# Kernel optimization log

Measured on AMD Instinct MI355X. Metric: run time of the kernel, lower is better.

Reference implementation:

```python
import jax, jax.numpy as jnp
import numpy as np

T, H, I, R, Z, K = 4096, 1024, 512, 32, 8, 4
E = R + Z
CAP = 768  # per-expert capacity; mean load = T*K/E = 409.6, CAP is ~18 sigma above mean


def setup_inputs() -> dict:
    key = jax.random.key(0)
    k1, k2, k3, k4, k5 = jax.random.split(key, 5)
    hidden_states = jax.random.normal(k1, (T, H), jnp.float32)
    top_k_index = jax.random.randint(k2, (T, K), 0, E).astype(jnp.int64)
    top_k_weights = jax.random.uniform(k3, (T, K), jnp.float32)
    gate_up_proj = jax.random.normal(k4, (E, 2 * I, H), jnp.float32) * 0.02
    down_proj = jax.random.normal(k5, (R, H, I), jnp.float32) * 0.02
    return {
        "hidden_states": hidden_states,
        "top_k_index": top_k_index,
        "top_k_weights": top_k_weights,
        "gate_up_proj": gate_up_proj,
        "down_proj": down_proj,
    }


def reference(hidden_states, top_k_index, top_k_weights, gate_up_proj, down_proj):
    n_tok, h = hidden_states.shape
    k = top_k_index.shape[1]
    n_routed = down_proj.shape[0]
    n_total = gate_up_proj.shape[0]
    A = n_tok * k  # total assignments

    flat_e = top_k_index.reshape(-1).astype(jnp.int32)          # [A]
    flat_t = jnp.repeat(jnp.arange(n_tok, dtype=jnp.int32), k)  # [A]
    flat_w = top_k_weights.reshape(-1)                          # [A]

    # ---- zero experts: weighted identity ----
    zero_w = jnp.sum(jnp.where(top_k_index >= n_routed, top_k_weights, 0.0), axis=1)
    out = hidden_states * zero_w[:, None]

    # ---- routed experts via capacity-buffer grouped GEMM ----
    order = jnp.argsort(flat_e)  # stable sort groups assignments by expert
    se = flat_e[order]
    st = flat_t[order]
    sw = flat_w[order]

    counts = jnp.bincount(flat_e, length=n_total)        # [E]
    starts = jnp.cumsum(counts) - counts                 # exclusive cumsum
    pos = jnp.arange(A, dtype=jnp.int32) - starts[se].astype(jnp.int32)  # slot within expert

    valid = (se < n_routed) & (pos < CAP)
    e_idx = jnp.where(valid, se, 0)
    p_idx = jnp.where(valid, pos, 0)

    xs = jnp.where(valid[:, None], hidden_states[st], 0.0)   # [A,H]
    xbuf = jnp.zeros((n_routed, CAP, h), hidden_states.dtype).at[e_idx, p_idx].add(xs)

    # grouped gated MLP: F.linear(x, W) == x @ W.T with W [out,in]
    gu = jnp.einsum('ech,eoh->eco', xbuf, gate_up_proj[:n_routed])  # [R,CAP,2I]
    gate, up = jnp.split(gu, 2, axis=-1)
    mid = jax.nn.silu(gate) * up                                    # [R,CAP,I]
    ybuf = jnp.einsum('eci,ehi->ech', mid, down_proj)               # [R,CAP,H]

    ya = ybuf[e_idx, p_idx] * jnp.where(valid, sw, 0.0)[:, None]    # [A,H]
    out = out.at[st].add(ya)
    return out
```

## Files before the change

kernel.cpp:

```cpp
#include <hip/hip_runtime.h>
#include <stdint.h>

#define NT 4096
#define HD 1024
#define ID 512
#define RE 32
#define EE 40
#define KT 4
#define CAPACITY 768

typedef __bf16 bf16x8 __attribute__((ext_vector_type(8)));
typedef float f32x4 __attribute__((ext_vector_type(4)));
typedef unsigned int u32x4 __attribute__((ext_vector_type(4)));
typedef unsigned int u32x2 __attribute__((ext_vector_type(2)));
typedef unsigned short u16x4 __attribute__((ext_vector_type(4)));

__device__ __forceinline__ float bf2f(unsigned short u) {
    union { unsigned int i; float f; } v; v.i = ((unsigned int)u) << 16; return v.f;
}
__device__ __forceinline__ unsigned short f2bf(float f) {
    union { float f; unsigned int i; } v; v.f = f;
    unsigned int u = v.i;
    return (unsigned short)((u + 0x7fffu + ((u >> 16) & 1u)) >> 16);
}

__device__ __forceinline__ u32x4 ld8(const void* p, size_t ei, int inF32) {
    if (!inF32) {
        return *(const u32x4*)((const unsigned short*)p + ei);
    } else {
        const float* f = (const float*)p + ei;
        f32x4 a = *(const f32x4*)f;
        f32x4 b = *(const f32x4*)(f + 4);
        u32x4 r;
        r[0] = (unsigned)f2bf(a[0]) | ((unsigned)f2bf(a[1]) << 16);
        r[1] = (unsigned)f2bf(a[2]) | ((unsigned)f2bf(a[3]) << 16);
        r[2] = (unsigned)f2bf(b[0]) | ((unsigned)f2bf(b[1]) << 16);
        r[3] = (unsigned)f2bf(b[2]) | ((unsigned)f2bf(b[3]) << 16);
        return r;
    }
}

typedef __attribute__((address_space(1))) const unsigned int gas_u32;
typedef __attribute__((address_space(3))) unsigned int las_u32;
#define GLL(g, l) __builtin_amdgcn_global_load_lds((gas_u32*)(g), (las_u32*)(l), 16, 0, 0)

__global__ __launch_bounds__(256) void detect_k(const void* __restrict__ X,
                                                const void* __restrict__ idx,
                                                int* __restrict__ flags) {
    __shared__ int sInsane, sOddNZ;
    const int tid = threadIdx.x;
    if (tid == 0) { sInsane = 0; sOddNZ = 0; }
    __syncthreads();
    const unsigned short* xu = (const unsigned short*)X;
    int cnt = 0;
    for (int i = tid; i < 8192; i += 256) {
        int e = (xu[i] >> 7) & 0xFF;
        if (e >= 0x90) cnt++;
    }
    if (cnt) atomicAdd(&sInsane, cnt);
    const int* ip = (const int*)idx;
    int odd = 0;
    for (int i = tid; i < 512; i += 256)
        if ((i & 1) && ip[i] != 0) odd++;
    if (odd) atomicAdd(&sOddNZ, odd);
    __syncthreads();
    if (tid == 0) {
        flags[0] = (sInsane > 64) ? 1 : 0;
        flags[1] = (sOddNZ == 0) ? 1 : 0;
    }
}

__global__ __launch_bounds__(256) void route_k(const int* __restrict__ idx,
                                               const void* __restrict__ wts,
                                               const int* __restrict__ flags,
                                               int* __restrict__ cnt,
                                               float* __restrict__ zw,
                                               int* __restrict__ tok,
                                               float* __restrict__ wslot,
                                               int* __restrict__ smap) {
    int a = blockIdx.x * 256 + threadIdx.x;
    if (a >= NT * KT) return;
    const int isI64 = flags[1];
    const int inF32 = flags[0];
    int e = isI64 ? idx[a << 1] : idx[a];
    float w = inF32 ? ((const float*)wts)[a] : bf2f(((const unsigned short*)wts)[a]);
    int s = -1;
    if (e < RE) {
        int slot = atomicAdd(&cnt[e], 1);
        if (slot < CAPACITY) {
            tok[e * CAPACITY + slot] = a >> 2;
            wslot[e * CAPACITY + slot] = w;
            s = slot;
        }
    } else {
        atomicAdd(&zw[a >> 2], w);
    }
    smap[a] = s;
}

__global__ __launch_bounds__(256) void convert_k(
    const void* __restrict__ X, const void* __restrict__ W1, const void* __restrict__ W2,
    const int* __restrict__ flags, const float* __restrict__ zw,
    unsigned short* __restrict__ Xb, unsigned short* __restrict__ W1b,
    unsigned short* __restrict__ W2b, float* __restrict__ out)
{
    const int inF32 = flags[0];
    const size_t gid = (size_t)blockIdx.x * 256 + threadIdx.x;
    const size_t stride = (size_t)gridDim.x * 256;
    const size_t nx = (size_t)NT * HD / 4;
    const size_t n1 = (size_t)RE * 2 * ID * HD / 4;
    const size_t n2 = (size_t)RE * HD * ID / 4;
    if (inF32) {
        for (size_t i = gid; i < nx; i += stride) {
            f32x4 v = ((const f32x4*)X)[i];
            u32x2 r; r[0] = (unsigned)f2bf(v[0]) | ((unsigned)f2bf(v[1]) << 16);
            r[1] = (unsigned)f2bf(v[2]) | ((unsigned)f2bf(v[3]) << 16);
            ((u32x2*)Xb)[i] = r;
            float z = zw[i >> 8];
            f32x4 o = {z * v[0], z * v[1], z * v[2], z * v[3]};
            ((f32x4*)out)[i] = o;
        }
        for (size_t i = gid; i < n1; i += stride) {
            f32x4 v = ((const f32x4*)W1)[i];
            u32x2 r; r[0] = (unsigned)f2bf(v[0]) | ((unsigned)f2bf(v[1]) << 16);
            r[1] = (unsigned)f2bf(v[2]) | ((unsigned)f2bf(v[3]) << 16);
            ((u32x2*)W1b)[i] = r;
        }
        for (size_t i = gid; i < n2; i += stride) {
            f32x4 v = ((const f32x4*)W2)[i];
            u32x2 r; r[0] = (unsigned)f2bf(v[0]) | ((unsigned)f2bf(v[1]) << 16);
            r[1] = (unsigned)f2bf(v[2]) | ((unsigned)f2bf(v[3]) << 16);
            ((u32x2*)W2b)[i] = r;
        }
    } else {
        for (size_t i = gid; i < nx; i += stride) {
            u32x2 r = ((const u32x2*)X)[i];
            ((u32x2*)Xb)[i] = r;
            float z = zw[i >> 8];
            f32x4 o = {z * bf2f((unsigned short)(r[0] & 0xffffu)),
                       z * bf2f((unsigned short)(r[0] >> 16)),
                       z * bf2f((unsigned short)(r[1] & 0xffffu)),
                       z * bf2f((unsigned short)(r[1] >> 16))};
            ((f32x4*)out)[i] = o;
        }
        for (size_t i = gid; i < n1; i += stride) ((u32x2*)W1b)[i] = ((const u32x2*)W1)[i];
        for (size_t i = gid; i < n2; i += stride) ((u32x2*)W2b)[i] = ((const u32x2*)W2)[i];
    }
}

__global__ __launch_bounds__(256, 2) void gemm1n_k(
    const unsigned short* __restrict__ Xb,
    const unsigned short* __restrict__ W1b,
    const int* __restrict__ cnts,
    const int* __restrict__ tok,
    unsigned short* __restrict__ mid)
{
    const int e = blockIdx.z;
    int cnt = cnts[e]; if (cnt > CAPACITY) cnt = CAPACITY;
    const int m0 = blockIdx.x * 128;
    if (m0 >= cnt) return;
    const int n0 = blockIdx.y * 128;

    __shared__ unsigned short Ash[3 * 4096];
    __shared__ unsigned short Bgs[3 * 4096];
    __shared__ unsigned short Bus[3 * 4096];

    const int tid  = threadIdx.x;
    const int lane = tid & 63;
    const int wv   = tid >> 6;
    const int wm   = wv >> 1, wn = wv & 1;
    const int q    = lane >> 4, ln = lane & 15;

    const int r0 = m0 + lane, r1 = m0 + 64 + lane;
    const int t0 = (r0 < cnt) ? tok[e * CAPACITY + r0] : 0;
    const int t1 = (r1 < cnt) ? tok[e * CAPACITY + r1] : 0;
    const unsigned short* gA0 = Xb + (size_t)t0 * HD + wv * 8;
    const unsigned short* gA1 = Xb + (size_t)t1 * HD + wv * 8;
    const unsigned short* gG0 = W1b + ((size_t)e * 1024 + n0 + lane) * HD + wv * 8;
    const unsigned short* gG1 = gG0 + (size_t)64 * HD;
    const unsigned short* gU0 = W1b + ((size_t)e * 1024 + 512 + n0 + lane) * HD + wv * 8;
    const unsigned short* gU1 = gU0 + (size_t)64 * HD;
    const int l0 = (wv * 128 + 0) * 8;
    const int l1 = (wv * 128 + 64) * 8;

    f32x4 accg[4][4], accu[4][4];
    const f32x4 z4 = {0.f, 0.f, 0.f, 0.f};
    #pragma unroll
    for (int a_ = 0; a_ < 4; a_++)
        #pragma unroll
        for (int b_ = 0; b_ < 4; b_++) { accg[a_][b_] = z4; accu[a_][b_] = z4; }

    #define STAGE1(k0, b) do { \
        GLL(gA0 + (k0), &Ash[(b) * 4096 + l0]); GLL(gA1 + (k0), &Ash[(b) * 4096 + l1]); \
        GLL(gG0 + (k0), &Bgs[(b) * 4096 + l0]); GLL(gG1 + (k0), &Bgs[(b) * 4096 + l1]); \
        GLL(gU0 + (k0), &Bus[(b) * 4096 + l0]); GLL(gU1 + (k0), &Bus[(b) * 4096 + l1]); } while (0)

    STAGE1(0, 0); STAGE1(32, 1); STAGE1(64, 2);

    int bsel = 0;
    for (int t = 0; t < 32; ++t) {
        if (t < 30)       asm volatile("s_waitcnt vmcnt(12)" ::: "memory");
        else if (t == 30) asm volatile("s_waitcnt vmcnt(6)" ::: "memory");
        else              asm volatile("s_waitcnt vmcnt(0)" ::: "memory");
        __builtin_amdgcn_s_barrier();
        __builtin_amdgcn_sched_barrier(0);
        const unsigned short* As = &Ash[bsel * 4096];
        const unsigned short* Gs = &Bgs[bsel * 4096];
        const unsigned short* Us = &Bus[bsel * 4096];
        bf16x8 af[4], bgf[4], buf2[4];
        #pragma unroll
        for (int mt = 0; mt < 4; mt++)
            af[mt] = *(const bf16x8*)&As[(q * 128 + wm * 64 + mt * 16 + ln) * 8];
        #pragma unroll
        for (int nt = 0; nt < 4; nt++) {
            bgf[nt]  = *(const bf16x8*)&Gs[(q * 128 + wn * 64 + nt * 16 + ln) * 8];
            buf2[nt] = *(const bf16x8*)&Us[(q * 128 + wn * 64 + nt * 16 + ln) * 8];
        }
        #pragma unroll
        for (int mt = 0; mt < 4; mt++)
            #pragma unroll
            for (int nt = 0; nt < 4; nt++) {
                accg[mt][nt] = __builtin_amdgcn_mfma_f32_16x16x32_bf16(af[mt], bgf[nt],  accg[mt][nt], 0, 0, 0);
                accu[mt][nt] = __builtin_amdgcn_mfma_f32_16x16x32_bf16(af[mt], buf2[nt], accu[mt][nt], 0, 0, 0);
            }
        asm volatile("s_waitcnt lgkmcnt(0)" ::: "memory");
        __builtin_amdgcn_sched_barrier(0);
        __builtin_amdgcn_s_barrier();
        __builtin_amdgcn_sched_barrier(0);
        if (t < 29) STAGE1((t + 3) * 32, bsel);
        bsel++; if (bsel == 3) bsel = 0;
    }
    #undef STAGE1

    const size_t midBase = (size_t)e * CAPACITY;
    #pragma unroll
    for (int mt = 0; mt < 4; mt++) {
        #pragma unroll
        for (int r = 0; r < 4; r++) {
            int slot = m0 + wm * 64 + mt * 16 + q * 4 + r;
            if (slot < cnt) {
                unsigned short* dst = mid + (midBase + slot) * ID;
                #pragma unroll
                for (int nt = 0; nt < 4; nt++) {
                    int i_col = n0 + wn * 64 + nt * 16 + ln;
                    float gv = accg[mt][nt][r];
                    float uv = accu[mt][nt][r];
                    float sv = gv / (1.f + __expf(-gv));
                    dst[i_col] = f2bf(sv * uv);
                }
            }
        }
    }
}

__global__ __launch_bounds__(256, 2) void gemm2n_k(
    const unsigned short* __restrict__ mid,
    const unsigned short* __restrict__ W2b,
    const int* __restrict__ cnts,
    const int* __restrict__ tok,
    const float* __restrict__ wslot,
    float* __restrict__ out)
{
    const int e = blockIdx.z;
    int cnt = cnts[e]; if (cnt > CAPACITY) cnt = CAPACITY;
    const int m0 = blockIdx.x * 128;
    if (m0 >= cnt) return;
    const int n0 = blockIdx.y * 128;

    __shared__ unsigned short Ash[3 * 4096];
    __shared__ unsigned short Bsh[3 * 4096];

    const int tid  = threadIdx.x;
    const int lane = tid & 63;
    const int wv   = tid >> 6;
    const int wm   = wv >> 1, wn = wv & 1;
    const int q    = lane >> 4, ln = lane & 15;

    const unsigned short* gA0 = mid + ((size_t)e * CAPACITY + m0 + lane) * ID + wv * 8;
    const unsigned short* gA1 = gA0 + (size_t)64 * ID;
    const unsigned short* gB0 = W2b + ((size_t)e * HD + n0 + lane) * ID + wv * 8;
    const unsigned short* gB1 = gB0 + (size_t)64 * ID;
    const int l0 = (wv * 128 + 0) * 8;
    const int l1 = (wv * 128 + 64) * 8;

    f32x4 acc[4][4];
    const f32x4 z4 = {0.f, 0.f, 0.f, 0.f};
    #pragma unroll
    for (int a_ = 0; a_ < 4; a_++)
        #pragma unroll
        for (int b_ = 0; b_ < 4; b_++) acc[a_][b_] = z4;

    #define STAGE2(k0, b) do { \
        GLL(gA0 + (k0), &Ash[(b) * 4096 + l0]); GLL(gA1 + (k0), &Ash[(b) * 4096 + l1]); \
        GLL(gB0 + (k0), &Bsh[(b) * 4096 + l0]); GLL(gB1 + (k0), &Bsh[(b) * 4096 + l1]); } while (0)

    STAGE2(0, 0); STAGE2(32, 1); STAGE2(64, 2);

    int bsel = 0;
    for (int t = 0; t < 16; ++t) {
        if (t < 14)       asm volatile("s_waitcnt vmcnt(8)" ::: "memory");
        else if (t == 14) asm volatile("s_waitcnt vmcnt(4)" ::: "memory");
        else              asm volatile("s_waitcnt vmcnt(0)" ::: "memory");
        __builtin_amdgcn_s_barrier();
        __builtin_amdgcn_sched_barrier(0);
        const unsigned short* As = &Ash[bsel * 4096];
        const unsigned short* Bs = &Bsh[bsel * 4096];
        bf16x8 af[4], bf[4];
        #pragma unroll
        for (int mt = 0; mt < 4; mt++)
            af[mt] = *(const bf16x8*)&As[(q * 128 + wm * 64 + mt * 16 + ln) * 8];
        #pragma unroll
        for (int nt = 0; nt < 4; nt++)
            bf[nt] = *(const bf16x8*)&Bs[(q * 128 + wn * 64 + nt * 16 + ln) * 8];
        #pragma unroll
        for (int mt = 0; mt < 4; mt++)
            #pragma unroll
            for (int nt = 0; nt < 4; nt++)
                acc[mt][nt] = __builtin_amdgcn_mfma_f32_16x16x32_bf16(af[mt], bf[nt], acc[mt][nt], 0, 0, 0);
        asm volatile("s_waitcnt lgkmcnt(0)" ::: "memory");
        __builtin_amdgcn_sched_barrier(0);
        __builtin_amdgcn_s_barrier();
        __builtin_amdgcn_sched_barrier(0);
        if (t < 13) STAGE2((t + 3) * 32, bsel);
        bsel++; if (bsel == 3) bsel = 0;
    }
    #undef STAGE2

    const int base = e * CAPACITY;
    #pragma unroll
    for (int mt = 0; mt < 4; mt++) {
        #pragma unroll
        for (int r = 0; r < 4; r++) {
            int slot = m0 + wm * 64 + mt * 16 + q * 4 + r;
            if (slot < cnt) {
                int tt = tok[base + slot];
                float w = wslot[base + slot];
                float* dst = out + (size_t)tt * HD + n0 + wn * 64 + ln;
                #pragma unroll
                for (int nt = 0; nt < 4; nt++)
                    atomicAdd(dst + nt * 16, w * acc[mt][nt][r]);
            }
        }
    }
}

__global__ __launch_bounds__(256, 2) void gemm1_k(
    const void* __restrict__ X, const void* __restrict__ W1,
    const int* __restrict__ flags, const int* __restrict__ cnts,
    const int* __restrict__ tok, unsigned short* __restrict__ mid)
{
    const int e = blockIdx.z;
    int cnt = cnts[e]; if (cnt > CAPACITY) cnt = CAPACITY;
    const int m0 = blockIdx.x * 128;
    if (m0 >= cnt) return;
    const int n0 = blockIdx.y * 128;
    const int inF32 = flags[0];

    __shared__ unsigned short Ash[4 * 128 * 8];
    __shared__ unsigned short Bgs[4 * 128 * 8];
    __shared__ unsigned short Bus[4 * 128 * 8];

    const int tid  = threadIdx.x;
    const int lane = tid & 63;
    const int wv   = tid >> 6;
    const int wm   = wv >> 1, wn = wv & 1;
    const int q    = lane >> 4, ln = lane & 15;
    const int row = tid & 127;
    const int kcb = tid >> 7;

    const int trow = (m0 + row < cnt) ? tok[e * CAPACITY + m0 + row] : 0;
    const size_t aOff = (size_t)trow * HD;
    const size_t gOff = ((size_t)e * 2 * ID + (n0 + row)) * HD;
    const size_t uOff = ((size_t)e * 2 * ID + (ID + n0 + row)) * HD;

    f32x4 accg[4][4], accu[4][4];
    const f32x4 z4 = {0.f, 0.f, 0.f, 0.f};
    #pragma unroll
    for (int a_ = 0; a_ < 4; a_++)
        #pragma unroll
        for (int b_ = 0; b_ < 4; b_++) { accg[a_][b_] = z4; accu[a_][b_] = z4; }

    u32x4 va[2], vg[2], vu[2];
    #pragma unroll
    for (int i = 0; i < 2; i++) {
        int kc = kcb + 2 * i;
        va[i] = ld8(X,  aOff + kc * 8, inF32);
        vg[i] = ld8(W1, gOff + kc * 8, inF32);
        vu[i] = ld8(W1, uOff + kc * 8, inF32);
    }

    for (int k0 = 0; k0 < HD; k0 += 32) {
        __syncthreads();
        #pragma unroll
        for (int i = 0; i < 2; i++) {
            int kc = kcb + 2 * i;
            *(u32x4*)&Ash[(kc * 128 + row) * 8] = va[i];
            *(u32x4*)&Bgs[(kc * 128 + row) * 8] = vg[i];
            *(u32x4*)&Bus[(kc * 128 + row) * 8] = vu[i];
        }
        __syncthreads();
        if (k0 + 32 < HD) {
            #pragma unroll
            for (int i = 0; i < 2; i++) {
                int kc = kcb + 2 * i;
                va[i] = ld8(X,  aOff + k0 + 32 + kc * 8, inF32);
                vg[i] = ld8(W1, gOff + k0 + 32 + kc * 8, inF32);
                vu[i] = ld8(W1, uOff + k0 + 32 + kc * 8, inF32);
            }
        }
        bf16x8 af[4], bgf[4], buf2[4];
        #pragma unroll
        for (int mt = 0; mt < 4; mt++)
            af[mt] = *(const bf16x8*)&Ash[(q * 128 + wm * 64 + mt * 16 + ln) * 8];
        #pragma unroll
        for (int nt = 0; nt < 4; nt++) {
            bgf[nt]  = *(const bf16x8*)&Bgs[(q * 128 + wn * 64 + nt * 16 + ln) * 8];
            buf2[nt] = *(const bf16x8*)&Bus[(q * 128 + wn * 64 + nt * 16 + ln) * 8];
        }
        #pragma unroll
        for (int mt = 0; mt < 4; mt++)
            #pragma unroll
            for (int nt = 0; nt < 4; nt++) {
                accg[mt][nt] = __builtin_amdgcn_mfma_f32_16x16x32_bf16(af[mt], bgf[nt],  accg[mt][nt], 0, 0, 0);
                accu[mt][nt] = __builtin_amdgcn_mfma_f32_16x16x32_bf16(af[mt], buf2[nt], accu[mt][nt], 0, 0, 0);
            }
    }

    const size_t midBase = (size_t)e * CAPACITY;
    #pragma unroll
    for (int mt = 0; mt < 4; mt++) {
        #pragma unroll
        for (int r = 0; r < 4; r++) {
            int slot = m0 + wm * 64 + mt * 16 + q * 4 + r;
            if (slot < cnt) {
                unsigned short* dst = mid + (midBase + slot) * ID;
                #pragma unroll
                for (int nt = 0; nt < 4; nt++) {
                    int i_col = n0 + wn * 64 + nt * 16 + ln;
                    float gv = accg[mt][nt][r];
                    float uv = accu[mt][nt][r];
                    float sv = gv / (1.f + __expf(-gv));
                    dst[i_col] = f2bf(sv * uv);
                }
            }
        }
    }
}

__global__ __launch_bounds__(256, 2) void gemm2_k(
    const unsigned short* __restrict__ mid, const void* __restrict__ W2,
    const int* __restrict__ flags, const int* __restrict__ cnts,
    unsigned short* __restrict__ ybuf)
{
    const int e = blockIdx.z;
    int cnt = cnts[e]; if (cnt > CAPACITY) cnt = CAPACITY;
    const int m0 = blockIdx.x * 128;
    if (m0 >= cnt) return;
    const int n0 = blockIdx.y * 128;
    const int inF32 = flags[0];

    __shared__ unsigned short Ash[4 * 128 * 8];
    __shared__ unsigned short Bsh[4 * 128 * 8];

    const int tid  = threadIdx.x;
    const int lane = tid & 63;
    const int wv   = tid >> 6;
    const int wm   = wv >> 1, wn = wv & 1;
    const int q    = lane >> 4, ln = lane & 15;
    const int row = tid & 127;
    const int kcb = tid >> 7;

    const unsigned short* aBase = mid + ((size_t)e * CAPACITY + m0 + row) * ID;
    const size_t bOff = ((size_t)e * HD + n0 + row) * ID;

    f32x4 acc[4][4];
    const f32x4 z4 = {0.f, 0.f, 0.f, 0.f};
    #pragma unroll
    for (int a_ = 0; a_ < 4; a_++)
        #pragma unroll
        for (int b_ = 0; b_ < 4; b_++) acc[a_][b_] = z4;

    u32x4 va[2], vb[2];
    #pragma unroll
    for (int i = 0; i < 2; i++) {
        int kc = kcb + 2 * i;
        va[i] = *(const u32x4*)(aBase + kc * 8);
        vb[i] = ld8(W2, bOff + kc * 8, inF32);
    }

    for (int k0 = 0; k0 < ID; k0 += 32) {
        __syncthreads();
        #pragma unroll
        for (int i = 0; i < 2; i++) {
            int kc = kcb + 2 * i;
            *(u32x4*)&Ash[(kc * 128 + row) * 8] = va[i];
            *(u32x4*)&Bsh[(kc * 128 + row) * 8] = vb[i];
        }
        __syncthreads();
        if (k0 + 32 < ID) {
            #pragma unroll
            for (int i = 0; i < 2; i++) {
                int kc = kcb + 2 * i;
                va[i] = *(const u32x4*)(aBase + k0 + 32 + kc * 8);
                vb[i] = ld8(W2, bOff + k0 + 32 + kc * 8, inF32);
            }
        }
        bf16x8 af[4], bf[4];
        #pragma unroll
        for (int mt = 0; mt < 4; mt++)
            af[mt] = *(const bf16x8*)&Ash[(q * 128 + wm * 64 + mt * 16 + ln) * 8];
        #pragma unroll
        for (int nt = 0; nt < 4; nt++)
            bf[nt] = *(const bf16x8*)&Bsh[(q * 128 + wn * 64 + nt * 16 + ln) * 8];
        #pragma unroll
        for (int mt = 0; mt < 4; mt++)
            #pragma unroll
            for (int nt = 0; nt < 4; nt++)
                acc[mt][nt] = __builtin_amdgcn_mfma_f32_16x16x32_bf16(af[mt], bf[nt], acc[mt][nt], 0, 0, 0);
    }

    const size_t yBase = (size_t)e * CAPACITY;
    #pragma unroll
    for (int mt = 0; mt < 4; mt++) {
        #pragma unroll
        for (int r = 0; r < 4; r++) {
            int slot = m0 + wm * 64 + mt * 16 + q * 4 + r;
            if (slot < cnt) {
                unsigned short* dst = ybuf + (yBase + slot) * HD;
                #pragma unroll
                for (int nt = 0; nt < 4; nt++) {
                    int h = n0 + wn * 64 + nt * 16 + ln;
                    dst[h] = f2bf(acc[mt][nt][r]);
                }
            }
        }
    }
}

__global__ __launch_bounds__(256) void gather_k(
    const void* __restrict__ X,
    const int* __restrict__ idx,
    const void* __restrict__ wts,
    const int* __restrict__ flags,
    const int* __restrict__ smap,
    const unsigned short* __restrict__ ybuf,
    float* __restrict__ out)
{
    const int t = blockIdx.x;
    const int tid = threadIdx.x;
    const int inF32 = flags[0];
    __shared__ int se[KT];
    __shared__ float sw[KT];
    __shared__ int ss[KT];
    if (tid < KT) {
        const int isI64 = flags[1];
        int a = t * KT + tid;
        se[tid] = isI64 ? idx[a << 1] : idx[a];
        sw[tid] = inF32 ? ((const float*)wts)[a] : bf2f(((const unsigned short*)wts)[a]);
        ss[tid] = smap[a];
    }
    __syncthreads();

    const int h = tid * 4;
    float x0, x1, x2, x3;
    if (inF32) {
        f32x4 xv = *(const f32x4*)((const float*)X + (size_t)t * HD + h);
        x0 = xv[0]; x1 = xv[1]; x2 = xv[2]; x3 = xv[3];
    } else {
        u16x4 xv = *(const u16x4*)((const unsigned short*)X + (size_t)t * HD + h);
        x0 = bf2f(xv[0]); x1 = bf2f(xv[1]); x2 = bf2f(xv[2]); x3 = bf2f(xv[3]);
    }
    float zw = 0.f;
    #pragma unroll
    for (int k = 0; k < KT; k++)
        if (se[k] >= RE) zw += sw[k];

    float a0 = zw * x0, a1 = zw * x1, a2 = zw * x2, a3 = zw * x3;

    #pragma unroll
    for (int k = 0; k < KT; k++) {
        if (se[k] < RE && ss[k] >= 0) {
            u16x4 yv = *(const u16x4*)&ybuf[((size_t)se[k] * CAPACITY + ss[k]) * HD + h];
            float w = sw[k];
            a0 += w * bf2f(yv[0]);
            a1 += w * bf2f(yv[1]);
            a2 += w * bf2f(yv[2]);
            a3 += w * bf2f(yv[3]);
        }
    }
    f32x4 o = {a0, a1, a2, a3};
    *(f32x4*)&out[(size_t)t * HD + h] = o;
}

extern "C" void kernel_launch(void* const* d_in, const int* in_sizes, int n_in,
                              void* d_out, int out_size, void* d_ws, size_t ws_size,
                              hipStream_t stream) {
    (void)in_sizes; (void)n_in; (void)out_size;
    const void* X   = d_in[0];
    const int*  idx = (const int*)d_in[1];
    const void* wts = d_in[2];
    const void* W1  = d_in[3];
    const void* W2  = d_in[4];
    float* out = (float*)d_out;

    char* ws = (char*)d_ws;
    const size_t OFF_CNT  = 128;
    const size_t OFF_ZW   = 256;
    const size_t OFF_TOK  = OFF_ZW + 16384;
    const size_t OFF_WSL  = OFF_TOK + 98304;
    const size_t OFF_SMAP = OFF_WSL + 98304;
    const size_t OFF_MID  = OFF_SMAP + 65536;
    const size_t MID_END  = OFF_MID + 25165824ull;
    const size_t OFF_W2B  = MID_END;
    const size_t OFF_XB   = OFF_W2B + 33554432ull;
    const size_t OFF_W1B  = OFF_XB + 8388608ull;
    const size_t NEED     = OFF_W1B + 67108864ull;

    int* flags = (int*)ws;
    int* cnt   = (int*)(ws + OFF_CNT);
    float* zw  = (float*)(ws + OFF_ZW);
    int* tok   = (int*)(ws + OFF_TOK);
    float* wsl = (float*)(ws + OFF_WSL);
    int* smap  = (int*)(ws + OFF_SMAP);
    unsigned short* mid = (unsigned short*)(ws + OFF_MID);

    hipMemsetAsync(ws, 0, OFF_ZW + 16384, stream);
    detect_k<<<dim3(1), dim3(256), 0, stream>>>(X, idx, flags);
    route_k<<<dim3(64), dim3(256), 0, stream>>>(idx, wts, flags, cnt, zw, tok, wsl, smap);

    if (ws_size >= NEED) {
        unsigned short* W2b = (unsigned short*)(ws + OFF_W2B);
        unsigned short* Xb  = (unsigned short*)(ws + OFF_XB);
        unsigned short* W1b = (unsigned short*)(ws + OFF_W1B);
        convert_k<<<dim3(2048), dim3(256), 0, stream>>>(X, W1, W2, flags, zw, Xb, W1b, W2b, out);
        gemm1n_k<<<dim3(6, 4, 32), dim3(256), 0, stream>>>(Xb, W1b, cnt, tok, mid);
        gemm2n_k<<<dim3(6, 8, 32), dim3(256), 0, stream>>>(mid, W2b, cnt, tok, wsl, out);
    } else {
        unsigned short* ybuf = (unsigned short*)(ws + MID_END);
        gemm1_k<<<dim3(6, 4, 32), dim3(256), 0, stream>>>(X, W1, flags, cnt, tok, mid);
        gemm2_k<<<dim3(6, 8, 32), dim3(256), 0, stream>>>(mid, W2, flags, cnt, ybuf);
        gather_k<<<dim3(4096), dim3(256), 0, stream>>>(X, idx, wts, flags, smap, ybuf, out);
    }
}
```

Baseline: 521.5 us.

## Pre-tile weights and intermediate into LDS-ready layout; replace atomic scatter with gather

The conversion kernel now writes W1, W2 and the intermediate activations in a tiled layout where each 32-wide k-slice of a 128-row tile is contiguous. This lets the global-to-LDS loads read contiguous 8 KB chunks instead of strided rows. The second GEMM no longer does weighted float atomicAdds into the output; it writes a bf16 ybuf, and a separate gather kernel combines the zero-expert identity term with the routed contributions. This adds a kernel launch and an extra ybuf round trip through memory, but removes contention on the atomics and the zero-weight atomics in routing. ybuf reuses the W1t region, which is safe because W1t is dead once gemm1 has finished.

```diff
diff --git a/kernel.cpp b/kernel.cpp
--- a/kernel.cpp
+++ b/kernel.cpp
@@ -44,6 +44,7 @@
 typedef __attribute__((address_space(3))) unsigned int las_u32;
 #define GLL(g, l) __builtin_amdgcn_global_load_lds((gas_u32*)(g), (las_u32*)(l), 16, 0, 0)
 
+
 __global__ __launch_bounds__(256) void detect_k(const void* __restrict__ X,
                                                 const void* __restrict__ idx,
                                                 int* __restrict__ flags) {
@@ -71,95 +72,70 @@
 }
 
 __global__ __launch_bounds__(256) void route_k(const int* __restrict__ idx,
-                                               const void* __restrict__ wts,
                                                const int* __restrict__ flags,
                                                int* __restrict__ cnt,
-                                               float* __restrict__ zw,
                                                int* __restrict__ tok,
-                                               float* __restrict__ wslot,
                                                int* __restrict__ smap) {
     int a = blockIdx.x * 256 + threadIdx.x;
     if (a >= NT * KT) return;
     const int isI64 = flags[1];
-    const int inF32 = flags[0];
     int e = isI64 ? idx[a << 1] : idx[a];
-    float w = inF32 ? ((const float*)wts)[a] : bf2f(((const unsigned short*)wts)[a]);
     int s = -1;
     if (e < RE) {
         int slot = atomicAdd(&cnt[e], 1);
         if (slot < CAPACITY) {
             tok[e * CAPACITY + slot] = a >> 2;
-            wslot[e * CAPACITY + slot] = w;
             s = slot;
         }
-    } else {
-        atomicAdd(&zw[a >> 2], w);
     }
     smap[a] = s;
 }
 
-__global__ __launch_bounds__(256) void convert_k(
+__global__ __launch_bounds__(256) void convertw_k(
     const void* __restrict__ X, const void* __restrict__ W1, const void* __restrict__ W2,
-    const int* __restrict__ flags, const float* __restrict__ zw,
-    unsigned short* __restrict__ Xb, unsigned short* __restrict__ W1b,
-    unsigned short* __restrict__ W2b, float* __restrict__ out)
+    const int* __restrict__ flags,
+    unsigned short* __restrict__ Xb, unsigned short* __restrict__ W1t,
+    unsigned short* __restrict__ W2t)
 {
     const int inF32 = flags[0];
     const size_t gid = (size_t)blockIdx.x * 256 + threadIdx.x;
     const size_t stride = (size_t)gridDim.x * 256;
-    const size_t nx = (size_t)NT * HD / 4;
-    const size_t n1 = (size_t)RE * 2 * ID * HD / 4;
-    const size_t n2 = (size_t)RE * HD * ID / 4;
-    if (inF32) {
-        for (size_t i = gid; i < nx; i += stride) {
-            f32x4 v = ((const f32x4*)X)[i];
-            u32x2 r; r[0] = (unsigned)f2bf(v[0]) | ((unsigned)f2bf(v[1]) << 16);
-            r[1] = (unsigned)f2bf(v[2]) | ((unsigned)f2bf(v[3]) << 16);
-            ((u32x2*)Xb)[i] = r;
-            float z = zw[i >> 8];
-            f32x4 o = {z * v[0], z * v[1], z * v[2], z * v[3]};
-            ((f32x4*)out)[i] = o;
-        }
-        for (size_t i = gid; i < n1; i += stride) {
-            f32x4 v = ((const f32x4*)W1)[i];
-            u32x2 r; r[0] = (unsigned)f2bf(v[0]) | ((unsigned)f2bf(v[1]) << 16);
-            r[1] = (unsigned)f2bf(v[2]) | ((unsigned)f2bf(v[3]) << 16);
-            ((u32x2*)W1b)[i] = r;
-        }
-        for (size_t i = gid; i < n2; i += stride) {
-            f32x4 v = ((const f32x4*)W2)[i];
-            u32x2 r; r[0] = (unsigned)f2bf(v[0]) | ((unsigned)f2bf(v[1]) << 16);
-            r[1] = (unsigned)f2bf(v[2]) | ((unsigned)f2bf(v[3]) << 16);
-            ((u32x2*)W2b)[i] = r;
-        }
-    } else {
-        for (size_t i = gid; i < nx; i += stride) {
-            u32x2 r = ((const u32x2*)X)[i];
-            ((u32x2*)Xb)[i] = r;
-            float z = zw[i >> 8];
-            f32x4 o = {z * bf2f((unsigned short)(r[0] & 0xffffu)),
-                       z * bf2f((unsigned short)(r[0] >> 16)),
-                       z * bf2f((unsigned short)(r[1] & 0xffffu)),
-                       z * bf2f((unsigned short)(r[1] >> 16))};
-            ((f32x4*)out)[i] = o;
-        }
-        for (size_t i = gid; i < n1; i += stride) ((u32x2*)W1b)[i] = ((const u32x2*)W1)[i];
-        for (size_t i = gid; i < n2; i += stride) ((u32x2*)W2b)[i] = ((const u32x2*)W2)[i];
-    }
-}
-
-__global__ __launch_bounds__(256, 2) void gemm1n_k(
+    const size_t nxc = (size_t)NT * HD / 8;
+    const size_t n1c = (size_t)RE * 8 * 32 * 4 * 128;
+    const size_t n2c = (size_t)RE * 8 * 16 * 4 * 128;
+    for (size_t c = gid; c < nxc; c += stride)
+        *(u32x4*)&Xb[c * 8] = ld8(X, c * 8, inF32);
+    for (size_t c = gid; c < n1c; c += stride) {
+        int row = (int)(c & 127);
+        size_t r1 = c >> 7;
+        int kc = (int)(r1 & 3); size_t r2 = r1 >> 2;
+        int kt = (int)(r2 & 31); size_t r3 = r2 >> 5;
+        size_t src = (r3 * 128 + row) * (size_t)HD + kt * 32 + kc * 8;
+        *(u32x4*)&W1t[c * 8] = ld8(W1, src, inF32);
+    }
+    for (size_t c = gid; c < n2c; c += stride) {
+        int row = (int)(c & 127);
+        size_t r1 = c >> 7;
+        int kc = (int)(r1 & 3); size_t r2 = r1 >> 2;
+        int kt = (int)(r2 & 15); size_t r3 = r2 >> 4;
+        size_t src = (r3 * 128 + row) * (size_t)ID + kt * 32 + kc * 8;
+        *(u32x4*)&W2t[c * 8] = ld8(W2, src, inF32);
+    }
+}
+
+__global__ __launch_bounds__(256, 2) void gemm1t_k(
     const unsigned short* __restrict__ Xb,
-    const unsigned short* __restrict__ W1b,
+    const unsigned short* __restrict__ W1t,
     const int* __restrict__ cnts,
     const int* __restrict__ tok,
-    unsigned short* __restrict__ mid)
+    unsigned short* __restrict__ midt)
 {
     const int e = blockIdx.z;
     int cnt = cnts[e]; if (cnt > CAPACITY) cnt = CAPACITY;
-    const int m0 = blockIdx.x * 128;
+    const int bx = blockIdx.x, by = blockIdx.y;
+    const int m0 = bx * 128;
     if (m0 >= cnt) return;
-    const int n0 = blockIdx.y * 128;
+    const int n0 = by * 128;
 
     __shared__ unsigned short Ash[3 * 4096];
     __shared__ unsigned short Bgs[3 * 4096];
@@ -176,10 +152,8 @@
     const int t1 = (r1 < cnt) ? tok[e * CAPACITY + r1] : 0;
     const unsigned short* gA0 = Xb + (size_t)t0 * HD + wv * 8;
     const unsigned short* gA1 = Xb + (size_t)t1 * HD + wv * 8;
-    const unsigned short* gG0 = W1b + ((size_t)e * 1024 + n0 + lane) * HD + wv * 8;
-    const unsigned short* gG1 = gG0 + (size_t)64 * HD;
-    const unsigned short* gU0 = W1b + ((size_t)e * 1024 + 512 + n0 + lane) * HD + wv * 8;
-    const unsigned short* gU1 = gU0 + (size_t)64 * HD;
+    const unsigned short* gT = W1t + (size_t)(e * 8 + by) * 32 * 4096 + (wv * 128 + lane) * 8;
+    const unsigned short* uT = W1t + (size_t)(e * 8 + 4 + by) * 32 * 4096 + (wv * 128 + lane) * 8;
     const int l0 = (wv * 128 + 0) * 8;
     const int l1 = (wv * 128 + 64) * 8;
 
@@ -190,12 +164,15 @@
         #pragma unroll
         for (int b_ = 0; b_ < 4; b_++) { accg[a_][b_] = z4; accu[a_][b_] = z4; }
 
-    #define STAGE1(k0, b) do { \
-        GLL(gA0 + (k0), &Ash[(b) * 4096 + l0]); GLL(gA1 + (k0), &Ash[(b) * 4096 + l1]); \
-        GLL(gG0 + (k0), &Bgs[(b) * 4096 + l0]); GLL(gG1 + (k0), &Bgs[(b) * 4096 + l1]); \
-        GLL(gU0 + (k0), &Bus[(b) * 4096 + l0]); GLL(gU1 + (k0), &Bus[(b) * 4096 + l1]); } while (0)
-
-    STAGE1(0, 0); STAGE1(32, 1); STAGE1(64, 2);
+    #define STAGE1(t, b) do { \
+        GLL(gA0 + (t) * 32,                &Ash[(b) * 4096 + l0]); \
+        GLL(gA1 + (t) * 32,                &Ash[(b) * 4096 + l1]); \
+        GLL(gT + (size_t)(t) * 4096,       &Bgs[(b) * 4096 + l0]); \
+        GLL(gT + (size_t)(t) * 4096 + 512, &Bgs[(b) * 4096 + l1]); \
+        GLL(uT + (size_t)(t) * 4096,       &Bus[(b) * 4096 + l0]); \
+        GLL(uT + (size_t)(t) * 4096 + 512, &Bus[(b) * 4096 + l1]); } while (0)
+
+    STAGE1(0, 0); STAGE1(1, 1); STAGE1(2, 2);
 
     int bsel = 0;
     for (int t = 0; t < 32; ++t) {
@@ -227,45 +204,44 @@
         __builtin_amdgcn_sched_barrier(0);
         __builtin_amdgcn_s_barrier();
         __builtin_amdgcn_sched_barrier(0);
-        if (t < 29) STAGE1((t + 3) * 32, bsel);
+        if (t < 29) STAGE1(t + 3, bsel);
         bsel++; if (bsel == 3) bsel = 0;
     }
     #undef STAGE1
 
-    const size_t midBase = (size_t)e * CAPACITY;
+    const size_t tbase = (size_t)(e * 6 + bx) * 16 * 4096;
     #pragma unroll
     for (int mt = 0; mt < 4; mt++) {
         #pragma unroll
         for (int r = 0; r < 4; r++) {
-            int slot = m0 + wm * 64 + mt * 16 + q * 4 + r;
-            if (slot < cnt) {
-                unsigned short* dst = mid + (midBase + slot) * ID;
+            int rowt = wm * 64 + mt * 16 + q * 4 + r;
+            if (m0 + rowt < cnt) {
                 #pragma unroll
                 for (int nt = 0; nt < 4; nt++) {
-                    int i_col = n0 + wn * 64 + nt * 16 + ln;
+                    int icol = n0 + wn * 64 + nt * 16 + ln;
                     float gv = accg[mt][nt][r];
                     float uv = accu[mt][nt][r];
                     float sv = gv / (1.f + __expf(-gv));
-                    dst[i_col] = f2bf(sv * uv);
+                    midt[tbase + (size_t)(icol >> 5) * 4096 +
+                         (((icol >> 3) & 3) * 128 + rowt) * 8 + (icol & 7)] = f2bf(sv * uv);
                 }
             }
         }
     }
 }
 
-__global__ __launch_bounds__(256, 2) void gemm2n_k(
-    const unsigned short* __restrict__ mid,
-    const unsigned short* __restrict__ W2b,
+__global__ __launch_bounds__(256, 3) void gemm2t_k(
+    const unsigned short* __restrict__ midt,
+    const unsigned short* __restrict__ W2t,
     const int* __restrict__ cnts,
-    const int* __restrict__ tok,
-    const float* __restrict__ wslot,
-    float* __restrict__ out)
+    unsigned short* __restrict__ ybuf)
 {
     const int e = blockIdx.z;
     int cnt = cnts[e]; if (cnt > CAPACITY) cnt = CAPACITY;
-    const int m0 = blockIdx.x * 128;
+    const int bx = blockIdx.x, by = blockIdx.y;
+    const int m0 = bx * 128;
     if (m0 >= cnt) return;
-    const int n0 = blockIdx.y * 128;
+    const int n0 = by * 128;
 
     __shared__ unsigned short Ash[3 * 4096];
     __shared__ unsigned short Bsh[3 * 4096];
@@ -276,10 +252,8 @@
     const int wm   = wv >> 1, wn = wv & 1;
     const int q    = lane >> 4, ln = lane & 15;
 
-    const unsigned short* gA0 = mid + ((size_t)e * CAPACITY + m0 + lane) * ID + wv * 8;
-    const unsigned short* gA1 = gA0 + (size_t)64 * ID;
-    const unsigned short* gB0 = W2b + ((size_t)e * HD + n0 + lane) * ID + wv * 8;
-    const unsigned short* gB1 = gB0 + (size_t)64 * ID;
+    const unsigned short* aT = midt + (size_t)(e * 6 + bx) * 16 * 4096 + (wv * 128 + lane) * 8;
+    const unsigned short* bT = W2t  + (size_t)(e * 8 + by) * 16 * 4096 + (wv * 128 + lane) * 8;
     const int l0 = (wv * 128 + 0) * 8;
     const int l1 = (wv * 128 + 64) * 8;
 
@@ -290,11 +264,13 @@
         #pragma unroll
         for (int b_ = 0; b_ < 4; b_++) acc[a_][b_] = z4;
 
-    #define STAGE2(k0, b) do { \
-        GLL(gA0 + (k0), &Ash[(b) * 4096 + l0]); GLL(gA1 + (k0), &Ash[(b) * 4096 + l1]); \
-        GLL(gB0 + (k0), &Bsh[(b) * 4096 + l0]); GLL(gB1 + (k0), &Bsh[(b) * 4096 + l1]); } while (0)
-
-    STAGE2(0, 0); STAGE2(32, 1); STAGE2(64, 2);
+    #define STAGE2(t, b) do { \
+        GLL(aT + (size_t)(t) * 4096,       &Ash[(b) * 4096 + l0]); \
+        GLL(aT + (size_t)(t) * 4096 + 512, &Ash[(b) * 4096 + l1]); \
+        GLL(bT + (size_t)(t) * 4096,       &Bsh[(b) * 4096 + l0]); \
+        GLL(bT + (size_t)(t) * 4096 + 512, &Bsh[(b) * 4096 + l1]); } while (0)
+
+    STAGE2(0, 0); STAGE2(1, 1); STAGE2(2, 2);
 
     int bsel = 0;
     for (int t = 0; t < 16; ++t) {
@@ -321,203 +297,10 @@
         __builtin_amdgcn_sched_barrier(0);
         __builtin_amdgcn_s_barrier();
         __builtin_amdgcn_sched_barrier(0);
-        if (t < 13) STAGE2((t + 3) * 32, bsel);
+        if (t < 13) STAGE2(t + 3, bsel);
         bsel++; if (bsel == 3) bsel = 0;
     }
     #undef STAGE2
-
-    const int base = e * CAPACITY;
-    #pragma unroll
-    for (int mt = 0; mt < 4; mt++) {
-        #pragma unroll
-        for (int r = 0; r < 4; r++) {
-            int slot = m0 + wm * 64 + mt * 16 + q * 4 + r;
-            if (slot < cnt) {
-                int tt = tok[base + slot];
-                float w = wslot[base + slot];
-                float* dst = out + (size_t)tt * HD + n0 + wn * 64 + ln;
-                #pragma unroll
-                for (int nt = 0; nt < 4; nt++)
-                    atomicAdd(dst + nt * 16, w * acc[mt][nt][r]);
-            }
-        }
-    }
-}
-
-__global__ __launch_bounds__(256, 2) void gemm1_k(
-    const void* __restrict__ X, const void* __restrict__ W1,
-    const int* __restrict__ flags, const int* __restrict__ cnts,
-    const int* __restrict__ tok, unsigned short* __restrict__ mid)
-{
-    const int e = blockIdx.z;
-    int cnt = cnts[e]; if (cnt > CAPACITY) cnt = CAPACITY;
-    const int m0 = blockIdx.x * 128;
-    if (m0 >= cnt) return;
-    const int n0 = blockIdx.y * 128;
-    const int inF32 = flags[0];
-
-    __shared__ unsigned short Ash[4 * 128 * 8];
-    __shared__ unsigned short Bgs[4 * 128 * 8];
-    __shared__ unsigned short Bus[4 * 128 * 8];
-
-    const int tid  = threadIdx.x;
-    const int lane = tid & 63;
-    const int wv   = tid >> 6;
-    const int wm   = wv >> 1, wn = wv & 1;
-    const int q    = lane >> 4, ln = lane & 15;
-    const int row = tid & 127;
-    const int kcb = tid >> 7;
-
-    const int trow = (m0 + row < cnt) ? tok[e * CAPACITY + m0 + row] : 0;
-    const size_t aOff = (size_t)trow * HD;
-    const size_t gOff = ((size_t)e * 2 * ID + (n0 + row)) * HD;
-    const size_t uOff = ((size_t)e * 2 * ID + (ID + n0 + row)) * HD;
-
-    f32x4 accg[4][4], accu[4][4];
-    const f32x4 z4 = {0.f, 0.f, 0.f, 0.f};
-    #pragma unroll
-    for (int a_ = 0; a_ < 4; a_++)
-        #pragma unroll
-        for (int b_ = 0; b_ < 4; b_++) { accg[a_][b_] = z4; accu[a_][b_] = z4; }
-
-    u32x4 va[2], vg[2], vu[2];
-    #pragma unroll
-    for (int i = 0; i < 2; i++) {
-        int kc = kcb + 2 * i;
-        va[i] = ld8(X,  aOff + kc * 8, inF32);
-        vg[i] = ld8(W1, gOff + kc * 8, inF32);
-        vu[i] = ld8(W1, uOff + kc * 8, inF32);
-    }
-
-    for (int k0 = 0; k0 < HD; k0 += 32) {
-        __syncthreads();
-        #pragma unroll
-        for (int i = 0; i < 2; i++) {
-            int kc = kcb + 2 * i;
-            *(u32x4*)&Ash[(kc * 128 + row) * 8] = va[i];
-            *(u32x4*)&Bgs[(kc * 128 + row) * 8] = vg[i];
-            *(u32x4*)&Bus[(kc * 128 + row) * 8] = vu[i];
-        }
-        __syncthreads();
-        if (k0 + 32 < HD) {
-            #pragma unroll
-            for (int i = 0; i < 2; i++) {
-                int kc = kcb + 2 * i;
-                va[i] = ld8(X,  aOff + k0 + 32 + kc * 8, inF32);
-                vg[i] = ld8(W1, gOff + k0 + 32 + kc * 8, inF32);
-                vu[i] = ld8(W1, uOff + k0 + 32 + kc * 8, inF32);
-            }
-        }
-        bf16x8 af[4], bgf[4], buf2[4];
-        #pragma unroll
-        for (int mt = 0; mt < 4; mt++)
-            af[mt] = *(const bf16x8*)&Ash[(q * 128 + wm * 64 + mt * 16 + ln) * 8];
-        #pragma unroll
-        for (int nt = 0; nt < 4; nt++) {
-            bgf[nt]  = *(const bf16x8*)&Bgs[(q * 128 + wn * 64 + nt * 16 + ln) * 8];
-            buf2[nt] = *(const bf16x8*)&Bus[(q * 128 + wn * 64 + nt * 16 + ln) * 8];
-        }
-        #pragma unroll
-        for (int mt = 0; mt < 4; mt++)
-            #pragma unroll
-            for (int nt = 0; nt < 4; nt++) {
-                accg[mt][nt] = __builtin_amdgcn_mfma_f32_16x16x32_bf16(af[mt], bgf[nt],  accg[mt][nt], 0, 0, 0);
-                accu[mt][nt] = __builtin_amdgcn_mfma_f32_16x16x32_bf16(af[mt], buf2[nt], accu[mt][nt], 0, 0, 0);
-            }
-    }
-
-    const size_t midBase = (size_t)e * CAPACITY;
-    #pragma unroll
-    for (int mt = 0; mt < 4; mt++) {
-        #pragma unroll
-        for (int r = 0; r < 4; r++) {
-            int slot = m0 + wm * 64 + mt * 16 + q * 4 + r;
-            if (slot < cnt) {
-                unsigned short* dst = mid + (midBase + slot) * ID;
-                #pragma unroll
-                for (int nt = 0; nt < 4; nt++) {
-                    int i_col = n0 + wn * 64 + nt * 16 + ln;
-                    float gv = accg[mt][nt][r];
-                    float uv = accu[mt][nt][r];
-                    float sv = gv / (1.f + __expf(-gv));
-                    dst[i_col] = f2bf(sv * uv);
-                }
-            }
-        }
-    }
-}
-
-__global__ __launch_bounds__(256, 2) void gemm2_k(
-    const unsigned short* __restrict__ mid, const void* __restrict__ W2,
-    const int* __restrict__ flags, const int* __restrict__ cnts,
-    unsigned short* __restrict__ ybuf)
-{
-    const int e = blockIdx.z;
-    int cnt = cnts[e]; if (cnt > CAPACITY) cnt = CAPACITY;
-    const int m0 = blockIdx.x * 128;
-    if (m0 >= cnt) return;
-    const int n0 = blockIdx.y * 128;
-    const int inF32 = flags[0];
-
-    __shared__ unsigned short Ash[4 * 128 * 8];
-    __shared__ unsigned short Bsh[4 * 128 * 8];
-
-    const int tid  = threadIdx.x;
-    const int lane = tid & 63;
-    const int wv   = tid >> 6;
-    const int wm   = wv >> 1, wn = wv & 1;
-    const int q    = lane >> 4, ln = lane & 15;
-    const int row = tid & 127;
-    const int kcb = tid >> 7;
-
-    const unsigned short* aBase = mid + ((size_t)e * CAPACITY + m0 + row) * ID;
-    const size_t bOff = ((size_t)e * HD + n0 + row) * ID;
-
-    f32x4 acc[4][4];
-    const f32x4 z4 = {0.f, 0.f, 0.f, 0.f};
-    #pragma unroll
-    for (int a_ = 0; a_ < 4; a_++)
-        #pragma unroll
-        for (int b_ = 0; b_ < 4; b_++) acc[a_][b_] = z4;
-
-    u32x4 va[2], vb[2];
-    #pragma unroll
-    for (int i = 0; i < 2; i++) {
-        int kc = kcb + 2 * i;
-        va[i] = *(const u32x4*)(aBase + kc * 8);
-        vb[i] = ld8(W2, bOff + kc * 8, inF32);
-    }
-
-    for (int k0 = 0; k0 < ID; k0 += 32) {
-        __syncthreads();
-        #pragma unroll
-        for (int i = 0; i < 2; i++) {
-            int kc = kcb + 2 * i;
-            *(u32x4*)&Ash[(kc * 128 + row) * 8] = va[i];
-            *(u32x4*)&Bsh[(kc * 128 + row) * 8] = vb[i];
-        }
-        __syncthreads();
-        if (k0 + 32 < ID) {
-            #pragma unroll
-            for (int i = 0; i < 2; i++) {
-                int kc = kcb + 2 * i;
-                va[i] = *(const u32x4*)(aBase + k0 + 32 + kc * 8);
-                vb[i] = ld8(W2, bOff + k0 + 32 + kc * 8, inF32);
-            }
-        }
-        bf16x8 af[4], bf[4];
-        #pragma unroll
-        for (int mt = 0; mt < 4; mt++)
-            af[mt] = *(const bf16x8*)&Ash[(q * 128 + wm * 64 + mt * 16 + ln) * 8];
-        #pragma unroll
-        for (int nt = 0; nt < 4; nt++)
-            bf[nt] = *(const bf16x8*)&Bsh[(q * 128 + wn * 64 + nt * 16 + ln) * 8];
-        #pragma unroll
-        for (int mt = 0; mt < 4; mt++)
-            #pragma unroll
-            for (int nt = 0; nt < 4; nt++)
-                acc[mt][nt] = __builtin_amdgcn_mfma_f32_16x16x32_bf16(af[mt], bf[nt], acc[mt][nt], 0, 0, 0);
-    }
 
     const size_t yBase = (size_t)e * CAPACITY;
     #pragma unroll
@@ -592,6 +375,199 @@
     *(f32x4*)&out[(size_t)t * HD + h] = o;
 }
 
+__global__ __launch_bounds__(256, 2) void gemm1_k(
+    const void* __restrict__ X, const void* __restrict__ W1,
+    const int* __restrict__ flags, const int* __restrict__ cnts,
+    const int* __restrict__ tok, unsigned short* __restrict__ mid)
+{
+    const int e = blockIdx.z;
+    int cnt = cnts[e]; if (cnt > CAPACITY) cnt = CAPACITY;
+    const int m0 = blockIdx.x * 128;
+    if (m0 >= cnt) return;
+    const int n0 = blockIdx.y * 128;
+    const int inF32 = flags[0];
+
+    __shared__ unsigned short Ash[4 * 128 * 8];
+    __shared__ unsigned short Bgs[4 * 128 * 8];
+    __shared__ unsigned short Bus[4 * 128 * 8];
+
+    const int tid  = threadIdx.x;
+    const int lane = tid & 63;
+    const int wv   = tid >> 6;
+    const int wm   = wv >> 1, wn = wv & 1;
+    const int q    = lane >> 4, ln = lane & 15;
+    const int row = tid & 127;
+    const int kcb = tid >> 7;
+
+    const int trow = (m0 + row < cnt) ? tok[e * CAPACITY + m0 + row] : 0;
+    const size_t aOff = (size_t)trow * HD;
+    const size_t gOff = ((size_t)e * 2 * ID + (n0 + row)) * HD;
+    const size_t uOff = ((size_t)e * 2 * ID + (ID + n0 + row)) * HD;
+
+    f32x4 accg[4][4], accu[4][4];
+    const f32x4 z4 = {0.f, 0.f, 0.f, 0.f};
+    #pragma unroll
+    for (int a_ = 0; a_ < 4; a_++)
+        #pragma unroll
+        for (int b_ = 0; b_ < 4; b_++) { accg[a_][b_] = z4; accu[a_][b_] = z4; }
+
+    u32x4 va[2], vg[2], vu[2];
+    #pragma unroll
+    for (int i = 0; i < 2; i++) {
+        int kc = kcb + 2 * i;
+        va[i] = ld8(X,  aOff + kc * 8, inF32);
+        vg[i] = ld8(W1, gOff + kc * 8, inF32);
+        vu[i] = ld8(W1, uOff + kc * 8, inF32);
+    }
+
+    for (int k0 = 0; k0 < HD; k0 += 32) {
+        __syncthreads();
+        #pragma unroll
+        for (int i = 0; i < 2; i++) {
+            int kc = kcb + 2 * i;
+            *(u32x4*)&Ash[(kc * 128 + row) * 8] = va[i];
+            *(u32x4*)&Bgs[(kc * 128 + row) * 8] = vg[i];
+            *(u32x4*)&Bus[(kc * 128 + row) * 8] = vu[i];
+        }
+        __syncthreads();
+        if (k0 + 32 < HD) {
+            #pragma unroll
+            for (int i = 0; i < 2; i++) {
+                int kc = kcb + 2 * i;
+                va[i] = ld8(X,  aOff + k0 + 32 + kc * 8, inF32);
+                vg[i] = ld8(W1, gOff + k0 + 32 + kc * 8, inF32);
+                vu[i] = ld8(W1, uOff + k0 + 32 + kc * 8, inF32);
+            }
+        }
+        bf16x8 af[4], bgf[4], buf2[4];
+        #pragma unroll
+        for (int mt = 0; mt < 4; mt++)
+            af[mt] = *(const bf16x8*)&Ash[(q * 128 + wm * 64 + mt * 16 + ln) * 8];
+        #pragma unroll
+        for (int nt = 0; nt < 4; nt++) {
+            bgf[nt]  = *(const bf16x8*)&Bgs[(q * 128 + wn * 64 + nt * 16 + ln) * 8];
+            buf2[nt] = *(const bf16x8*)&Bus[(q * 128 + wn * 64 + nt * 16 + ln) * 8];
+        }
+        #pragma unroll
+        for (int mt = 0; mt < 4; mt++)
+            #pragma unroll
+            for (int nt = 0; nt < 4; nt++) {
+                accg[mt][nt] = __builtin_amdgcn_mfma_f32_16x16x32_bf16(af[mt], bgf[nt],  accg[mt][nt], 0, 0, 0);
+                accu[mt][nt] = __builtin_amdgcn_mfma_f32_16x16x32_bf16(af[mt], buf2[nt], accu[mt][nt], 0, 0, 0);
+            }
+    }
+
+    const size_t midBase = (size_t)e * CAPACITY;
+    #pragma unroll
+    for (int mt = 0; mt < 4; mt++) {
+        #pragma unroll
+        for (int r = 0; r < 4; r++) {
+            int slot = m0 + wm * 64 + mt * 16 + q * 4 + r;
+            if (slot < cnt) {
+                unsigned short* dst = mid + (midBase + slot) * ID;
+                #pragma unroll
+                for (int nt = 0; nt < 4; nt++) {
+                    int i_col = n0 + wn * 64 + nt * 16 + ln;
+                    float gv = accg[mt][nt][r];
+                    float uv = accu[mt][nt][r];
+                    float sv = gv / (1.f + __expf(-gv));
+                    dst[i_col] = f2bf(sv * uv);
+                }
+            }
+        }
+    }
+}
+
+__global__ __launch_bounds__(256, 2) void gemm2_k(
+    const unsigned short* __restrict__ mid, const void* __restrict__ W2,
+    const int* __restrict__ flags, const int* __restrict__ cnts,
+    unsigned short* __restrict__ ybuf)
+{
+    const int e = blockIdx.z;
+    int cnt = cnts[e]; if (cnt > CAPACITY) cnt = CAPACITY;
+    const int m0 = blockIdx.x * 128;
+    if (m0 >= cnt) return;
+    const int n0 = blockIdx.y * 128;
+    const int inF32 = flags[0];
+
+    __shared__ unsigned short Ash[4 * 128 * 8];
+    __shared__ unsigned short Bsh[4 * 128 * 8];
+
+    const int tid  = threadIdx.x;
+    const int lane = tid & 63;
+    const int wv   = tid >> 6;
+    const int wm   = wv >> 1, wn = wv & 1;
+    const int q    = lane >> 4, ln = lane & 15;
+    const int row = tid & 127;
+    const int kcb = tid >> 7;
+
+    const unsigned short* aBase = mid + ((size_t)e * CAPACITY + m0 + row) * ID;
+    const size_t bOff = ((size_t)e * HD + n0 + row) * ID;
+
+    f32x4 acc[4][4];
+    const f32x4 z4 = {0.f, 0.f, 0.f, 0.f};
+    #pragma unroll
+    for (int a_ = 0; a_ < 4; a_++)
+        #pragma unroll
+        for (int b_ = 0; b_ < 4; b_++) acc[a_][b_] = z4;
+
+    u32x4 va[2], vb[2];
+    #pragma unroll
+    for (int i = 0; i < 2; i++) {
+        int kc = kcb + 2 * i;
+        va[i] = *(const u32x4*)(aBase + kc * 8);
+        vb[i] = ld8(W2, bOff + kc * 8, inF32);
+    }
+
+    for (int k0 = 0; k0 < ID; k0 += 32) {
+        __syncthreads();
+        #pragma unroll
+        for (int i = 0; i < 2; i++) {
+            int kc = kcb + 2 * i;
+            *(u32x4*)&Ash[(kc * 128 + row) * 8] = va[i];
+            *(u32x4*)&Bsh[(kc * 128 + row) * 8] = vb[i];
+        }
+        __syncthreads();
+        if (k0 + 32 < ID) {
+            #pragma unroll
+            for (int i = 0; i < 2; i++) {
+                int kc = kcb + 2 * i;
+                va[i] = *(const u32x4*)(aBase + k0 + 32 + kc * 8);
+                vb[i] = ld8(W2, bOff + k0 + 32 + kc * 8, inF32);
+            }
+        }
+        bf16x8 af[4], bf[4];
+        #pragma unroll
+        for (int mt = 0; mt < 4; mt++)
+            af[mt] = *(const bf16x8*)&Ash[(q * 128 + wm * 64 + mt * 16 + ln) * 8];
+        #pragma unroll
+        for (int nt = 0; nt < 4; nt++)
+            bf[nt] = *(const bf16x8*)&Bsh[(q * 128 + wn * 64 + nt * 16 + ln) * 8];
+        #pragma unroll
+        for (int mt = 0; mt < 4; mt++)
+            #pragma unroll
+            for (int nt = 0; nt < 4; nt++)
+                acc[mt][nt] = __builtin_amdgcn_mfma_f32_16x16x32_bf16(af[mt], bf[nt], acc[mt][nt], 0, 0, 0);
+    }
+
+    const size_t yBase = (size_t)e * CAPACITY;
+    #pragma unroll
+    for (int mt = 0; mt < 4; mt++) {
+        #pragma unroll
+        for (int r = 0; r < 4; r++) {
+            int slot = m0 + wm * 64 + mt * 16 + q * 4 + r;
+            if (slot < cnt) {
+                unsigned short* dst = ybuf + (yBase + slot) * HD;
+                #pragma unroll
+                for (int nt = 0; nt < 4; nt++) {
+                    int h = n0 + wn * 64 + nt * 16 + ln;
+                    dst[h] = f2bf(acc[mt][nt][r]);
+                }
+            }
+        }
+    }
+}
+
 extern "C" void kernel_launch(void* const* d_in, const int* in_sizes, int n_in,
                               void* d_out, int out_size, void* d_ws, size_t ws_size,
                               hipStream_t stream) {
@@ -605,38 +581,36 @@
 
     char* ws = (char*)d_ws;
     const size_t OFF_CNT  = 128;
-    const size_t OFF_ZW   = 256;
-    const size_t OFF_TOK  = OFF_ZW + 16384;
-    const size_t OFF_WSL  = OFF_TOK + 98304;
-    const size_t OFF_SMAP = OFF_WSL + 98304;
+    const size_t OFF_TOK  = 256;
+    const size_t OFF_SMAP = OFF_TOK + 98304;
     const size_t OFF_MID  = OFF_SMAP + 65536;
-    const size_t MID_END  = OFF_MID + 25165824ull;
-    const size_t OFF_W2B  = MID_END;
-    const size_t OFF_XB   = OFF_W2B + 33554432ull;
-    const size_t OFF_W1B  = OFF_XB + 8388608ull;
-    const size_t NEED     = OFF_W1B + 67108864ull;
+    const size_t OFF_W2T  = OFF_MID + 25165824ull;
+    const size_t OFF_XB   = OFF_W2T + 33554432ull;
+    const size_t OFF_W1T  = OFF_XB + 8388608ull;
+    const size_t NEED     = OFF_W1T + 67108864ull;
 
     int* flags = (int*)ws;
     int* cnt   = (int*)(ws + OFF_CNT);
-    float* zw  = (float*)(ws + OFF_ZW);
     int* tok   = (int*)(ws + OFF_TOK);
-    float* wsl = (float*)(ws + OFF_WSL);
     int* smap  = (int*)(ws + OFF_SMAP);
-    unsigned short* mid = (unsigned short*)(ws + OFF_MID);
-
-    hipMemsetAsync(ws, 0, OFF_ZW + 16384, stream);
+
+    hipMemsetAsync(ws, 0, 256, stream);
     detect_k<<<dim3(1), dim3(256), 0, stream>>>(X, idx, flags);
-    route_k<<<dim3(64), dim3(256), 0, stream>>>(idx, wts, flags, cnt, zw, tok, wsl, smap);
+    route_k<<<dim3(64), dim3(256), 0, stream>>>(idx, flags, cnt, tok, smap);
 
     if (ws_size >= NEED) {
-        unsigned short* W2b = (unsigned short*)(ws + OFF_W2B);
-        unsigned short* Xb  = (unsigned short*)(ws + OFF_XB);
-        unsigned short* W1b = (unsigned short*)(ws + OFF_W1B);
-        convert_k<<<dim3(2048), dim3(256), 0, stream>>>(X, W1, W2, flags, zw, Xb, W1b, W2b, out);
-        gemm1n_k<<<dim3(6, 4, 32), dim3(256), 0, stream>>>(Xb, W1b, cnt, tok, mid);
-        gemm2n_k<<<dim3(6, 8, 32), dim3(256), 0, stream>>>(mid, W2b, cnt, tok, wsl, out);
+        unsigned short* midt = (unsigned short*)(ws + OFF_MID);
+        unsigned short* W2t  = (unsigned short*)(ws + OFF_W2T);
+        unsigned short* Xb   = (unsigned short*)(ws + OFF_XB);
+        unsigned short* W1t  = (unsigned short*)(ws + OFF_W1T);
+        unsigned short* ybuf = (unsigned short*)(ws + OFF_W1T);
+        convertw_k<<<dim3(2048), dim3(256), 0, stream>>>(X, W1, W2, flags, Xb, W1t, W2t);
+        gemm1t_k<<<dim3(6, 4, 32), dim3(256), 0, stream>>>(Xb, W1t, cnt, tok, midt);
+        gemm2t_k<<<dim3(6, 8, 32), dim3(256), 0, stream>>>(midt, W2t, cnt, ybuf);
+        gather_k<<<dim3(4096), dim3(256), 0, stream>>>(X, idx, wts, flags, smap, ybuf, out);
     } else {
-        unsigned short* ybuf = (unsigned short*)(ws + MID_END);
+        unsigned short* mid  = (unsigned short*)(ws + OFF_MID);
+        unsigned short* ybuf = (unsigned short*)(ws + OFF_W2T);
         gemm1_k<<<dim3(6, 4, 32), dim3(256), 0, stream>>>(X, W1, flags, cnt, tok, mid);
         gemm2_k<<<dim3(6, 8, 32), dim3(256), 0, stream>>>(mid, W2, flags, cnt, ybuf);
         gather_k<<<dim3(4096), dim3(256), 0, stream>>>(X, idx, wts, flags, smap, ybuf, out);
```

Result: faster. 507.6 us (-2.7%).
